# Performance work log

Measured on AMD Instinct MI355X. Metric: run time of the kernel, lower is better.

Reference implementation:

```python
import jax, jax.numpy as jnp
import numpy as np

N = 75000      # nodes
E = 1200000    # edges
D = 64         # in_channels == out_channels (residual add)
H = 64         # hidden_channels
G = 64         # graphs in batch
DROP = 0.1


def setup_inputs() -> dict:
    key = jax.random.key(0)
    ks = jax.random.split(key, 6)
    x = jax.random.normal(ks[0], (N, D), dtype=jnp.float32)
    edge_index = jax.random.randint(ks[1], (2, E), 0, N, dtype=jnp.int32)
    edge_attr = jax.random.uniform(ks[2], (E, 2), dtype=jnp.float32)
    batch = jnp.sort(jax.random.randint(ks[3], (N,), 0, G, dtype=jnp.int32))
    # deterministic drop-edge mask: exactly floor((1-DROP)*E) kept, shuffled
    num_keep = int((1 - DROP) * E)
    mask = np.zeros(E, dtype=bool)
    mask[:num_keep] = True
    np.random.default_rng(0).shuffle(mask)
    keep_mask = jnp.asarray(mask)
    W1 = jax.random.normal(ks[4], (D, H), dtype=jnp.float32) / np.float32(np.sqrt(D))
    b1 = jnp.zeros((H,), dtype=jnp.float32)
    W2 = jax.random.normal(ks[5], (H, D), dtype=jnp.float32) / np.float32(np.sqrt(H))
    b2 = jnp.zeros((D,), dtype=jnp.float32)
    return dict(x=x, edge_index=edge_index, edge_attr=edge_attr, batch=batch,
                keep_mask=keep_mask, W1=W1, b1=b1, W2=W2, b2=b2)


def gcn_conv(x, W, b, row, col, ew, n):
    """GCNConv with weighted edges and self-loops (weight 1).
    out_i = sum_j norm_ij * (x_j W) + dinv_i^2 * (x_i W) + b
    norm_ij = deg_i^-1/2 * w_ij * deg_j^-1/2, deg = sum of incident weights + 1."""
    xw = x @ W                                            # [n, out]
    deg = jax.ops.segment_sum(ew, col, num_segments=n) + 1.0
    dinv = jax.lax.rsqrt(deg)                             # [n]
    norm = dinv[row] * ew * dinv[col]                     # [E]
    out = jax.ops.segment_sum(xw[row] * norm[:, None], col, num_segments=n)
    out = out + xw * (dinv * dinv)[:, None]               # self-loop term
    return out + b


def reference(x, edge_index, edge_attr, batch, keep_mask, W1, b1, W2, b2):
    row, col = edge_index[0], edge_index[1]
    w = edge_attr[:, 1]
    wmax, wmin = w.max(), w.min()
    ew = (wmax - w) / (wmax - wmin)                       # normalize_weight (inverted)
    h = x
    ew_drop = jnp.where(keep_mask, ew, 0.0)               # drop_edge == zero weight
    x1 = jax.nn.relu(gcn_conv(x, W1, b1, row, col, ew_drop, N))
    x2 = gcn_conv(x1, W2, b2, row, col, ew, N) + h        # residual
    return jax.ops.segment_max(x2, batch, num_segments=G) # global_max_pool -> [G, D]
```

## Files before the change

kernel.cpp:

```cpp
#include <hip/hip_runtime.h>
#include <hip/hip_bf16.h>

__device__ __forceinline__ unsigned fmap(float f) {
    unsigned b = __float_as_uint(f);
    return (b & 0x80000000u) ? ~b : (b | 0x80000000u);
}
__device__ __forceinline__ float funmap(unsigned u) {
    unsigned b = (u & 0x80000000u) ? (u & 0x7FFFFFFFu) : ~u;
    return __uint_as_float(b);
}

__global__ void k_zero(unsigned* __restrict__ z, int nwords, unsigned* __restrict__ mm) {
    int i = blockIdx.x * blockDim.x + threadIdx.x;
    int stride = gridDim.x * blockDim.x;
    for (; i < nwords; i += stride) z[i] = 0u;
    if (blockIdx.x == 0 && threadIdx.x == 0) {
        mm[0] = 0u;
        mm[1] = 0xFFFFFFFFu;
    }
}

__global__ void k_maskdet(const unsigned char* __restrict__ m, int nbytes, int* __restrict__ flag) {
    __shared__ int s[256];
    int t = threadIdx.x;
    int cnt = 0;
    for (int i = t; i < nbytes; i += 256) cnt += (m[i] != 0);
    s[t] = cnt;
    __syncthreads();
    for (int d = 128; d > 0; d >>= 1) {
        if (t < d) s[t] += s[t + d];
        __syncthreads();
    }
    if (t == 0) flag[0] = (2 * s[0] > nbytes) ? 1 : 0;
}

__global__ void k_minmax(const float* __restrict__ attr, unsigned* __restrict__ mm, int E) {
    float lmin = 1e30f, lmax = -1e30f;
    for (int i = blockIdx.x * blockDim.x + threadIdx.x; i < E; i += gridDim.x * blockDim.x) {
        float w = attr[2 * i + 1];
        lmin = fminf(lmin, w);
        lmax = fmaxf(lmax, w);
    }
    #pragma unroll
    for (int o = 32; o > 0; o >>= 1) {
        lmin = fminf(lmin, __shfl_down(lmin, o));
        lmax = fmaxf(lmax, __shfl_down(lmax, o));
    }
    if ((threadIdx.x & 63) == 0) {
        atomicMax(mm + 0, fmap(lmax));
        atomicMin(mm + 1, fmap(lmin));
    }
}

__global__ void k_slot(const int* __restrict__ ei, int* __restrict__ cur,
                       int* __restrict__ rel, int E) {
    int i = blockIdx.x * blockDim.x + threadIdx.x;
    if (i >= E) return;
    int col = ei[E + i];
    rel[i] = atomicAdd(cur + col, 1);
}

__global__ __launch_bounds__(512) void k_scan_part(const int* __restrict__ in, int* __restrict__ out,
                                                   int* __restrict__ sums, int n) {
    __shared__ int s[512];
    int t = threadIdx.x;
    int i = blockIdx.x * 512 + t;
    int v = (i < n) ? in[i] : 0;
    s[t] = v;
    __syncthreads();
    for (int d = 1; d < 512; d <<= 1) {
        int x = (t >= d) ? s[t - d] : 0;
        __syncthreads();
        s[t] += x;
        __syncthreads();
    }
    if (i < n) out[i] = s[t] - v;
    if (t == 511) sums[blockIdx.x] = s[511];
}
__global__ __launch_bounds__(256) void k_scan_mid(int* __restrict__ sums, int n) {
    __shared__ int s[256];
    int t = threadIdx.x;
    int v = (t < n) ? sums[t] : 0;
    s[t] = v;
    __syncthreads();
    for (int d = 1; d < 256; d <<= 1) {
        int x = (t >= d) ? s[t - d] : 0;
        __syncthreads();
        s[t] += x;
        __syncthreads();
    }
    if (t < n) sums[t] = s[t] - v;
}
__global__ __launch_bounds__(512) void k_scan_add(int* __restrict__ out, const int* __restrict__ sums, int n) {
    int i = blockIdx.x * 512 + threadIdx.x;
    if (i < n) out[i] += sums[blockIdx.x];
}

__global__ void k_scatter(const int* __restrict__ ei, const float* __restrict__ attr,
                          const unsigned char* __restrict__ maskb, const int* __restrict__ maski,
                          const int* __restrict__ mflag, const unsigned* __restrict__ mm,
                          const int* __restrict__ off, const int* __restrict__ rel,
                          int2* __restrict__ csr, int E) {
    int i = blockIdx.x * blockDim.x + threadIdx.x;
    if (i >= E) return;
    float wmax = funmap(mm[0]);
    float wmin = funmap(mm[1]);
    float w = attr[2 * i + 1];
    float v = (wmax - w) / (wmax - wmin);
    bool keep = mflag[0] ? (maskb[i] != 0) : (maski[i] != 0);
    float stored = keep ? v : -v;
    int col = ei[E + i];
    int p = off[col] + rel[i];
    csr[p] = make_int2(ei[i], __float_as_int(stored));
}

__global__ void k_deg(const int2* __restrict__ csr,
                      const int* __restrict__ off, const int* __restrict__ cnt,
                      float* __restrict__ dinv1, float* __restrict__ dinv2, int N) {
    int i = blockIdx.x * blockDim.x + threadIdx.x;
    if (i >= N) return;
    int s = off[i], c = cnt[i];
    float a = 0.0f, b = 0.0f;
    for (int j = 0; j < c; j++) {
        float v = __int_as_float(csr[s + j].y);
        a += fmaxf(v, 0.0f);
        b += fabsf(v);
    }
    dinv1[i] = 1.0f / sqrtf(a + 1.0f);
    dinv2[i] = 1.0f / sqrtf(b + 1.0f);
}

__global__ __launch_bounds__(256) void k_gemm(const float* __restrict__ X, const float* __restrict__ W,
                                              float* __restrict__ Y, const float* __restrict__ sc, int n) {
    __shared__ float xs[64][68];
    __shared__ float ws[64 * 64];
    int t = threadIdx.x;
    int rowBase = blockIdx.x * 64;
    #pragma unroll
    for (int j = 0; j < 4; j++) {
        int f = t + 256 * j;
        reinterpret_cast<float4*>(ws)[f] = reinterpret_cast<const float4*>(W)[f];
    }
    #pragma unroll
    for (int j = 0; j < 4; j++) {
        int f = t + 256 * j;
        int r = f >> 4, c4 = (f & 15) << 2;
        float4 v = make_float4(0.f, 0.f, 0.f, 0.f);
        if (rowBase + r < n)
            v = *reinterpret_cast<const float4*>(X + (size_t)(rowBase + r) * 64 + c4);
        *reinterpret_cast<float4*>(&xs[r][c4]) = v;
    }
    __syncthreads();
    int c0 = (t & 15) << 2;
    int r0 = (t >> 4) << 2;
    float acc[4][4] = {};
    #pragma unroll
    for (int k0 = 0; k0 < 64; k0 += 4) {
        float4 xr[4], wv[4];
        #pragma unroll
        for (int rr = 0; rr < 4; rr++)
            xr[rr] = *reinterpret_cast<const float4*>(&xs[r0 + rr][k0]);
        #pragma unroll
        for (int kk = 0; kk < 4; kk++)
            wv[kk] = *reinterpret_cast<const float4*>(&ws[(k0 + kk) * 64 + c0]);
        #pragma unroll
        for (int rr = 0; rr < 4; rr++) {
            const float* xp = reinterpret_cast<const float*>(&xr[rr]);
            #pragma unroll
            for (int kk = 0; kk < 4; kk++) {
                const float a = xp[kk];
                const float* wp = reinterpret_cast<const float*>(&wv[kk]);
                #pragma unroll
                for (int cc = 0; cc < 4; cc++)
                    acc[rr][cc] = fmaf(a, wp[cc], acc[rr][cc]);
            }
        }
    }
    #pragma unroll
    for (int rr = 0; rr < 4; rr++) {
        int r = rowBase + r0 + rr;
        if (r < n) {
            float s = sc[r];
            float4 o = make_float4(acc[rr][0] * s, acc[rr][1] * s, acc[rr][2] * s, acc[rr][3] * s);
            *reinterpret_cast<float4*>(Y + (size_t)r * 64 + c0) = o;
        }
    }
}

template <int LAYER>
__global__ __launch_bounds__(256) void k_gather(const float* __restrict__ xw, const float* __restrict__ dinv,
                                                const int* __restrict__ off, const int* __restrict__ cnt,
                                                const int2* __restrict__ csr,
                                                const float* __restrict__ bias, const float* __restrict__ xres,
                                                const int* __restrict__ batch, float* __restrict__ out,
                                                unsigned* __restrict__ seg, int N) {
    int wid = threadIdx.x >> 6;
    int lane = threadIdx.x & 63;
    int i = blockIdx.x * 4 + wid;
    if (i >= N) return;
    int s = off[i];
    int c = cnt[i];
    float di = dinv[i];
    float self = xw[(size_t)i * 64 + lane];
    float acc = 0.0f;
    for (int base = 0; base < c; base += 64) {
        int m = min(64, c - base);
        int r = 0;
        float w = 0.0f;
        if (lane < m) {
            int2 e = csr[s + base + lane];
            r = e.x;
            float sv = __int_as_float(e.y);
            w = (LAYER == 1) ? fmaxf(sv, 0.0f) : fabsf(sv);
        }
        #pragma unroll 4
        for (int j = 0; j < m; j++) {
            int rj = __shfl(r, j);
            float wj = __shfl(w, j);
            acc = fmaf(wj, xw[(size_t)rj * 64 + lane], acc);
        }
    }
    float v = fmaf(di, acc + self, bias[lane]);
    if (LAYER == 1) {
        out[(size_t)i * 64 + lane] = fmaxf(v, 0.0f);
    } else {
        v += xres[(size_t)i * 64 + lane];
        int g = batch[i];
        atomicMax(seg + g * 64 + lane, fmap(v));
    }
}

__global__ void k_out(const unsigned* __restrict__ seg, float* __restrict__ out, int n) {
    int i = blockIdx.x * blockDim.x + threadIdx.x;
    if (i < n) out[i] = funmap(seg[i]);
}

extern "C" void kernel_launch(void* const* d_in, const int* in_sizes, int n_in,
                              void* d_out, int out_size, void* d_ws, size_t ws_size,
                              hipStream_t stream) {
    const float* x             = (const float*)d_in[0];
    const int* ei              = (const int*)d_in[1];
    const float* attr          = (const float*)d_in[2];
    const int* batch           = (const int*)d_in[3];
    const unsigned char* maskb = (const unsigned char*)d_in[4];
    const int* maski           = (const int*)d_in[4];
    const float* W1            = (const float*)d_in[5];
    const float* b1            = (const float*)d_in[6];
    const float* W2            = (const float*)d_in[7];
    const float* b2            = (const float*)d_in[8];

    const int N = in_sizes[3];
    const int E = in_sizes[4];

    size_t cur_off = 0;
    auto alloc = [&](size_t bytes) -> char* {
        cur_off = (cur_off + 255) & ~(size_t)255;
        char* p = (char*)d_ws + cur_off;
        cur_off += bytes;
        return p;
    };
    int2* csr      = (int2*)alloc((size_t)E * 8);
    int* rel       = (int*)alloc((size_t)E * 4);
    int* curp      = (int*)alloc((size_t)N * 4);
    unsigned* seg  = (unsigned*)alloc((size_t)out_size * 4);
    char* zero_end = (char*)d_ws + cur_off;
    unsigned* mm   = (unsigned*)alloc(2 * 4);
    int* mflag     = (int*)alloc(4);
    int* offa      = (int*)alloc((size_t)N * 4);
    int* sums      = (int*)alloc(256 * 4);
    float* dinv1   = (float*)alloc((size_t)N * 4);
    float* dinv2   = (float*)alloc((size_t)N * 4);
    float* xw      = (float*)alloc((size_t)N * 64 * 4);
    float* x1      = (float*)alloc((size_t)N * 64 * 4);

    int zwords = (int)((zero_end - (char*)curp) / 4);

    const int B = 256;
    int nblkE = (E + B - 1) / B;
    int nblkN = (N + B - 1) / B;
    int nblkScan = (N + 511) / 512;
    int nblkGemm = (N + 63) / 64;
    int nblkGather = (N + 3) / 4;
    int detBytes = (E < 65536) ? E : 65536;

    k_zero<<<128, B, 0, stream>>>((unsigned*)curp, zwords, mm);
    k_maskdet<<<1, 256, 0, stream>>>(maskb, detBytes, mflag);
    k_minmax<<<512, B, 0, stream>>>(attr, mm, E);
    k_slot<<<nblkE, B, 0, stream>>>(ei, curp, rel, E);
    k_scan_part<<<nblkScan, 512, 0, stream>>>(curp, offa, sums, N);
    k_scan_mid<<<1, 256, 0, stream>>>(sums, nblkScan);
    k_scan_add<<<nblkScan, 512, 0, stream>>>(offa, sums, N);
    k_scatter<<<nblkE, B, 0, stream>>>(ei, attr, maskb, maski, mflag, mm, offa, rel, csr, E);
    k_deg<<<nblkN, B, 0, stream>>>(csr, offa, curp, dinv1, dinv2, N);

    k_gemm<<<nblkGemm, B, 0, stream>>>(x, W1, xw, dinv1, N);
    k_gather<1><<<nblkGather, B, 0, stream>>>(xw, dinv1, offa, curp, csr, b1,
                                              nullptr, batch, x1, nullptr, N);
    k_gemm<<<nblkGemm, B, 0, stream>>>(x1, W2, xw, dinv2, N);
    k_gather<2><<<nblkGather, B, 0, stream>>>(xw, dinv2, offa, curp, csr, b2,
                                              x, batch, nullptr, seg, N);
    k_out<<<(out_size + B - 1) / B, B, 0, stream>>>(seg, (float*)d_out, out_size);
}
```

Baseline: 567.2 us.

## Split wavefront into four edge groups with float4 row gathers in GCN gather

The gather kernel now splits each 64-lane wavefront into four 16-lane groups. Each group handles a different edge and loads a full 64-float source row as float4 per lane, and the partial sums are combined with xor shuffles at the end. This replaces one edge at a time with per-edge shuffles of index and weight, cutting shuffle overhead and putting four independent row loads in flight per iteration. In exchange it adds a reduction step, leaves lanes idle on the last iteration when the degree is not a multiple of four, and has only a quarter of the lanes doing the epilogue.

```diff
diff --git a/kernel.cpp b/kernel.cpp
--- a/kernel.cpp
+++ b/kernel.cpp
@@ -201,32 +201,50 @@
     int s = off[i];
     int c = cnt[i];
     float di = dinv[i];
-    float self = xw[(size_t)i * 64 + lane];
-    float acc = 0.0f;
-    for (int base = 0; base < c; base += 64) {
-        int m = min(64, c - base);
+    int e = lane >> 4;
+    int q = lane & 15;
+    float4 acc = make_float4(0.f, 0.f, 0.f, 0.f);
+    #pragma unroll 2
+    for (int base = 0; base < c; base += 4) {
+        int idx = base + e;
         int r = 0;
         float w = 0.0f;
-        if (lane < m) {
-            int2 e = csr[s + base + lane];
-            r = e.x;
-            float sv = __int_as_float(e.y);
+        if (idx < c) {
+            int2 ed = csr[s + idx];
+            r = ed.x;
+            float sv = __int_as_float(ed.y);
             w = (LAYER == 1) ? fmaxf(sv, 0.0f) : fabsf(sv);
         }
-        #pragma unroll 4
-        for (int j = 0; j < m; j++) {
-            int rj = __shfl(r, j);
-            float wj = __shfl(w, j);
-            acc = fmaf(wj, xw[(size_t)rj * 64 + lane], acc);
+        float4 xv = *reinterpret_cast<const float4*>(xw + (size_t)r * 64 + (q << 2));
+        acc.x = fmaf(w, xv.x, acc.x);
+        acc.y = fmaf(w, xv.y, acc.y);
+        acc.z = fmaf(w, xv.z, acc.z);
+        acc.w = fmaf(w, xv.w, acc.w);
+    }
+    acc.x += __shfl_xor(acc.x, 16); acc.y += __shfl_xor(acc.y, 16);
+    acc.z += __shfl_xor(acc.z, 16); acc.w += __shfl_xor(acc.w, 16);
+    acc.x += __shfl_xor(acc.x, 32); acc.y += __shfl_xor(acc.y, 32);
+    acc.z += __shfl_xor(acc.z, 32); acc.w += __shfl_xor(acc.w, 32);
+    if (e == 0) {
+        float4 self = *reinterpret_cast<const float4*>(xw + (size_t)i * 64 + (q << 2));
+        float4 b4   = *reinterpret_cast<const float4*>(bias + (q << 2));
+        float4 v;
+        v.x = fmaf(di, acc.x + self.x, b4.x);
+        v.y = fmaf(di, acc.y + self.y, b4.y);
+        v.z = fmaf(di, acc.z + self.z, b4.z);
+        v.w = fmaf(di, acc.w + self.w, b4.w);
+        if (LAYER == 1) {
+            float4 o = make_float4(fmaxf(v.x, 0.f), fmaxf(v.y, 0.f), fmaxf(v.z, 0.f), fmaxf(v.w, 0.f));
+            *reinterpret_cast<float4*>(out + (size_t)i * 64 + (q << 2)) = o;
+        } else {
+            float4 xr = *reinterpret_cast<const float4*>(xres + (size_t)i * 64 + (q << 2));
+            int g = batch[i];
+            unsigned* sp = seg + g * 64 + (q << 2);
+            atomicMax(sp + 0, fmap(v.x + xr.x));
+            atomicMax(sp + 1, fmap(v.y + xr.y));
+            atomicMax(sp + 2, fmap(v.z + xr.z));
+            atomicMax(sp + 3, fmap(v.w + xr.w));
         }
-    }
-    float v = fmaf(di, acc + self, bias[lane]);
-    if (LAYER == 1) {
-        out[(size_t)i * 64 + lane] = fmaxf(v, 0.0f);
-    } else {
-        v += xres[(size_t)i * 64 + lane];
-        int g = batch[i];
-        atomicMax(seg + g * 64 + lane, fmap(v));
     }
 }
 
```

New measurement: 787.0 us. +38.8%, slower.
